# Performance work log

Hardware: AMD Instinct MI355X
Metric: run time of the kernel (lower is better)

## Reference

```python
import jax, jax.numpy as jnp
import numpy as np
from jax import lax

BS, L, D = 512, 200, 128
N_SKILL, N_DIFF, N_HINTS, N_TIME = 1000, 100, 10, 50


def setup_inputs() -> dict:
    key = jax.random.key(0)
    ks = jax.random.split(key, 32)
    s = 1.0 / np.sqrt(D)
    f = jnp.float32
    inp = {
        'skill': jax.random.randint(ks[0], (BS, L), 0, N_SKILL),
        'answer': jax.random.randint(ks[1], (BS, L), 0, 2),
        'diff': jax.random.randint(ks[2], (BS, L), 0, N_DIFF),
        'hints': jax.random.randint(ks[3], (BS, L), 0, N_HINTS),
        'time_used': jax.random.randint(ks[4], (BS, L), 0, N_TIME),
        # embedding tables (padding rows left random; indices never hit them)
        'skill_emb': jax.random.normal(ks[5], (N_SKILL + 2, D), f),
        'answer_emb': jax.random.normal(ks[6], (3, D), f),
        'diff_emb': jax.random.normal(ks[7], (N_DIFF + 2, D), f),
        'hints_emb': jax.random.normal(ks[8], (N_HINTS + 2, D), f),
        'time_emb': jax.random.normal(ks[9], (N_TIME + 2, D), f),
        # Linear weights stored as (in, out): y = x @ W + b
        'Wq2': jax.random.normal(ks[10], (D, D), f) * s,
        'Wk2': jax.random.normal(ks[11], (D, D), f) * s,
        'Wv2': jax.random.normal(ks[12], (D, D), f) * s,
        'Wq3': jax.random.normal(ks[13], (D, D), f) * s,
        'Wk3': jax.random.normal(ks[14], (D, D), f) * s,
        'Wv3': jax.random.normal(ks[15], (D, D), f) * s,
        'fc_W': jax.random.normal(ks[16], (2 * D, D), f) * s,
        'fc_b': jax.random.normal(ks[17], (D,), f) * 0.01,
        'fc2_W': jax.random.normal(ks[18], (2 * D, D), f) * s,
        'fc2_b': jax.random.normal(ks[19], (D,), f) * 0.01,
        'f11_W': jax.random.normal(ks[20], (D, D), f) * s,
        'f11_b': jax.random.normal(ks[21], (D,), f) * 0.01,
        'f12_W': jax.random.normal(ks[22], (D, D), f) * s,
        'f12_b': jax.random.normal(ks[23], (D,), f) * 0.01,
        'f21_W': jax.random.normal(ks[24], (D, D), f) * s,
        'f21_b': jax.random.normal(ks[25], (D,), f) * 0.01,
        'f22_W': jax.random.normal(ks[26], (D, D), f) * s,
        'f22_b': jax.random.normal(ks[27], (D,), f) * 0.01,
    }
    return inp


def _forward(skill, answer, diff, hints, time_used,
             skill_emb, answer_emb, diff_emb, hints_emb, time_emb,
             Wq2, Wk2, Wv2, Wq3, Wk3, Wv3,
             fc_W, fc_b, fc2_W, fc2_b,
             f11_W, f11_b, f12_W, f12_b, f21_W, f21_b, f22_W, f22_b):
    bs = skill.shape[0]
    inv = jnp.asarray(1.0 / np.sqrt(D), skill_emb.dtype)
    es = skill_emb[skill]          # [bs, L, D]
    ed = diff_emb[diff]
    ea = answer_emb[answer]
    eh = hints_emb[hints]
    eu = time_emb[time_used]
    x = jnp.concatenate([es, ed], -1) @ fc_W + fc_b   # [bs, L, D]

    # time-major slices for scan: [L-1, bs, D]
    xs = jnp.swapaxes(x[:, :-1, :], 0, 1)
    xn = jnp.swapaxes(x[:, 1:, :], 0, 1)
    u_t = jnp.swapaxes(eu[:, :-1, :], 0, 1)
    h_t = jnp.swapaxes(eh[:, :-1, :], 0, 1)
    a_t = jnp.swapaxes(ea[:, :-1, :], 0, 1)

    def step(carry, inp):
        h, c = carry
        x_t, x_next, used_t, hints_t, at = inp
        x_t = jnp.concatenate([x_t, h], -1) @ fc2_W + fc2_b
        # branch 1 (W_q_1/W_k_1/W_v_1, used_t) is dead code in the original:
        # out = out_1 + out_2 is immediately overwritten by out = out_2.
        q2 = x_t @ Wq2
        k2 = c @ Wk2
        v2 = hints_t @ Wv2
        out = v2 * jax.nn.sigmoid(q2 * k2 * inv)
        c = jnp.tanh(out @ f11_W + f11_b) * jax.nn.sigmoid(out @ f12_W + f12_b) + c
        q3 = x_t @ Wk3   # note: original swaps W_k_3/W_q_3 names here
        k3 = h @ Wq3
        v3 = at @ Wv3
        o3 = v3 * jax.nn.sigmoid(q3 * k3 * inv)
        h = jnp.tanh(o3 @ f21_W + f21_b) * jax.nn.sigmoid(o3 @ f22_W + f22_b) + c
        y = jax.nn.sigmoid(jnp.sum(x_next * h, axis=-1))  # [bs]
        return (h, c), y

    h0 = jnp.zeros((bs, D), x.dtype)
    c0 = jnp.zeros((bs, D), x.dtype)
    _, ys = lax.scan(step, (h0, c0), (xs, xn, u_t, h_t, a_t))  # ys: [L-1, bs]
    y_pred = jnp.concatenate([ys.T, jnp.zeros((bs, 1), x.dtype)], axis=1)  # [bs, L]
    return y_pred


def reference(skill, answer, diff, hints, time_used,
              skill_emb, answer_emb, diff_emb, hints_emb, time_emb,
              Wq2, Wk2, Wv2, Wq3, Wk3, Wv3,
              fc_W, fc_b, fc2_W, fc2_b,
              f11_W, f11_b, f12_W, f12_b, f21_W, f21_b, f22_W, f22_b):
    return _forward(skill, answer, diff, hints, time_used,
                    skill_emb, answer_emb, diff_emb, hints_emb, time_emb,
                    Wq2, Wk2, Wv2, Wq3, Wk3, Wv3,
                    fc_W, fc_b, fc2_W, fc2_b,
                    f11_W, f11_b, f12_W, f12_b, f21_W, f21_b, f22_W, f22_b)
```

## Files before the change

### kernel.cpp

```cpp
#include <hip/hip_runtime.h>
#include <stdint.h>

typedef unsigned short u16;
typedef unsigned char u8;
typedef unsigned int u32;
typedef unsigned long long u64;

using h8f  = __attribute__((ext_vector_type(8))) _Float16;
using f4_t = __attribute__((ext_vector_type(4))) float;
using l2_t = __attribute__((ext_vector_type(2))) long;

#define MFMAH(a,b,c)  __builtin_amdgcn_mfma_f32_16x16x32_f16((a),(b),(c),0,0,0)
#define MFMAF8(a,b,c) __builtin_amdgcn_mfma_f32_16x16x32_fp8_fp8((a),(b),(c),0,0,0)

#define LO_SCALE 4096.0f
#define LO_INV   0.000244140625f

__device__ __forceinline__ float sigm(float x) {
  return __builtin_amdgcn_rcpf(1.f + __expf(-x));
}
__device__ __forceinline__ float tanh_f(float x) {
  x = fminf(30.f, fmaxf(-30.f, x));
  float e = __expf(-2.f * x);
  return (1.f - e) * __builtin_amdgcn_rcpf(1.f + e);
}
__device__ __forceinline__ u16 f2h_bits(float f) {
  _Float16 h = (_Float16)f;
  union { _Float16 h; u16 u; } v; v.h = h; return v.u;
}
__device__ __forceinline__ float h2f(u16 u) {
  union { _Float16 h; u16 u; } v; v.u = u; return (float)v.h;
}
__device__ __forceinline__ u32 pkrtz(float a, float b) {
  union { __attribute__((ext_vector_type(2))) __fp16 h; u32 u; } v;
  v.h = __builtin_amdgcn_cvt_pkrtz(a, b);
  return v.u;
}
__device__ __forceinline__ u32 pk4f8(float a, float b, float c, float d) {
  u32 r = 0;
  r = __builtin_amdgcn_cvt_pk_fp8_f32(a, b, (int)r, false);
  r = __builtin_amdgcn_cvt_pk_fp8_f32(c, d, (int)r, true);
  return r;
}


__global__ void k_gemm128(const float* __restrict__ A, const float* __restrict__ B,
                          float* __restrict__ C) {
  int g = blockIdx.x * 256 + threadIdx.x;
  int row = g >> 5;
  int c0 = (g & 31) << 2;
  f4_t acc = {0.f, 0.f, 0.f, 0.f};
  for (int k = 0; k < 128; ++k) {
    float a = A[row * 128 + k];
    acc += a * *(const f4_t*)&B[k * 128 + c0];
  }
  *(f4_t*)&C[row * 128 + c0] = acc;
}

__global__ void k_wbig(const float* __restrict__ fc_W, const float* __restrict__ B2,
                       const float* __restrict__ B3, float* __restrict__ WB) {
  int g = blockIdx.x * 256 + threadIdx.x;
  int row = g / 96;
  int j0 = (g % 96) * 4;
  if (j0 < 128) {
    *(f4_t*)&WB[row * 384 + j0] = *(const f4_t*)&fc_W[row * 128 + j0];
  } else {
    const float* Bm = (j0 < 256) ? B2 : B3;
    int jj = j0 & 127;
    f4_t acc = {0.f, 0.f, 0.f, 0.f};
    for (int n = 0; n < 128; ++n)
      acc += fc_W[row * 128 + n] * *(const f4_t*)&Bm[n * 128 + jj];
    *(f4_t*)&WB[row * 384 + j0] = acc;
  }
}

__global__ void k_bbig(const float* __restrict__ fc_b, const float* __restrict__ fc2_b,
                       const float* __restrict__ B2, const float* __restrict__ B3,
                       const float* __restrict__ Wq2, const float* __restrict__ Wk3,
                       float* __restrict__ bb) {
  int j = blockIdx.x * 256 + threadIdx.x;
  if (j >= 384) return;
  if (j < 128) { bb[j] = fc_b[j]; return; }
  const float* Bm = (j < 256) ? B2 : B3;
  const float* Wm = (j < 256) ? Wq2 : Wk3;
  int jj = j & 127;
  float acc = 0.f;
  for (int n = 0; n < 128; ++n)
    acc += fc_b[n] * Bm[n * 128 + jj] + fc2_b[n] * Wm[n * 128 + jj];
  bb[j] = acc;
}

__global__ void k_skdf(const float* __restrict__ skill_emb, const float* __restrict__ diff_emb,
                       const float* __restrict__ WB, const float* __restrict__ bb,
                       float* __restrict__ SK, float* __restrict__ DF) {
  int g = blockIdx.x * 256 + threadIdx.x;
  int row = g / 96, j0 = (g % 96) * 4;
  if (blockIdx.y == 0) {
    if (row >= 1002) return;
    f4_t acc = {0.f, 0.f, 0.f, 0.f};
    for (int d = 0; d < 128; ++d)
      acc += skill_emb[row * 128 + d] * *(const f4_t*)&WB[d * 384 + j0];
    *(f4_t*)&SK[row * 384 + j0] = acc;
  } else {
    if (row >= 102) return;
    f4_t acc = *(const f4_t*)&bb[j0];
    for (int d = 0; d < 128; ++d)
      acc += diff_emb[row * 128 + d] * *(const f4_t*)&WB[(128 + d) * 384 + j0];
    *(f4_t*)&DF[row * 384 + j0] = acc;
  }
}

__global__ void k_tv(const float* __restrict__ hints_emb, const float* __restrict__ Wv2,
                     const float* __restrict__ answer_emb, const float* __restrict__ Wv3,
                     float* __restrict__ Tv2, float* __restrict__ Tv3) {
  int g = blockIdx.x * 256 + threadIdx.x;
  if (g < 384) {
    int i = g >> 5, j0 = (g & 31) << 2;
    f4_t acc = {0.f, 0.f, 0.f, 0.f};
    for (int d = 0; d < 128; ++d)
      acc += hints_emb[i * 128 + d] * *(const f4_t*)&Wv2[d * 128 + j0];
    *(f4_t*)&Tv2[i * 128 + j0] = acc;
  } else if (g < 480) {
    int g2 = g - 384;
    int i = g2 >> 5, j0 = (g2 & 31) << 2;
    f4_t acc = {0.f, 0.f, 0.f, 0.f};
    for (int d = 0; d < 128; ++d)
      acc += answer_emb[i * 128 + d] * *(const f4_t*)&Wv3[d * 128 + j0];
    *(f4_t*)&Tv3[i * 128 + j0] = acc;
  }
}

struct P8 { const float* p[8]; };
__global__ void k_pack(P8 s, u16* __restrict__ whi, u8* __restrict__ wl8) {
  int g = blockIdx.x * 256 + threadIdx.x;
  bool lo = (g >= 16384);
  int gg = g & 16383;
  int m = gg >> 11;
  int r = gg & 2047;
  int ct = (r >> 10) & 1, kk = (r >> 8) & 3, wv = (r >> 6) & 3, l = r & 63;
  const float* src = s.p[m];
  int col = wv * 32 + ct * 16 + (l & 15);
  int kbase = kk * 32 + ((l >> 4) << 3);
  if (!lo) {
    u16 o[8];
    #pragma unroll
    for (int e = 0; e < 8; ++e) o[e] = f2h_bits(src[(kbase + e) * 128 + col]);
    uint4 u;
    u.x = o[0] | ((u32)o[1] << 16); u.y = o[2] | ((u32)o[3] << 16);
    u.z = o[4] | ((u32)o[5] << 16); u.w = o[6] | ((u32)o[7] << 16);
    *(uint4*)(whi + gg * 8) = u;
  } else {
    float lv[8];
    #pragma unroll
    for (int e = 0; e < 8; ++e) {
      float v = src[(kbase + e) * 128 + col];
      lv[e] = (v - (float)((_Float16)v)) * LO_SCALE;
    }
    uint2 u;
    u.x = pk4f8(lv[0], lv[1], lv[2], lv[3]);
    u.y = pk4f8(lv[4], lv[5], lv[6], lv[7]);
    *(uint2*)(wl8 + (size_t)gg * 8) = u;
  }
}


#define RSTRIDE 136
#define RS8 272

__launch_bounds__(256, 1)
__global__ void k_main(const int* __restrict__ skill, const int* __restrict__ answer,
                       const int* __restrict__ diff, const int* __restrict__ hints,
                       const float* __restrict__ SK, const float* __restrict__ DF,
                       const float* __restrict__ Tv2, const float* __restrict__ Tv3,
                       const u16* __restrict__ whi, const u8* __restrict__ wl8,
                       const float* __restrict__ b11p, const float* __restrict__ b12p,
                       const float* __restrict__ b21p, const float* __restrict__ b22p,
                       float* __restrict__ out) {
  __shared__ u16 sh_h[16 * RSTRIDE], sh_hl[16 * RSTRIDE];
  __shared__ u16 sh_c[16 * RSTRIDE], sh_cl[16 * RSTRIDE];
  __shared__ u16 sh_o[16 * RSTRIDE], sh_ol[16 * RSTRIDE];
  __shared__ u16 sh_o3[16 * RSTRIDE], sh_o3l[16 * RSTRIDE];
  __shared__ u8 sh_hc8[16 * RS8];
  __shared__ u8 sh_oo8[16 * RS8];
  __shared__ float sh_red[64];

  const int tid = threadIdx.x;
  const int w = tid >> 6, lane = tid & 63;
  const int row = lane & 15;
  const int fgrp = lane >> 4;
  const int f0a = w * 32 + fgrp * 4;
  const int f0b = f0a + 16;
  const int row_g = blockIdx.x * 16 + row;
  const int r200 = row_g * 200;

  h8f  WH[8][2][4];
  long WL[8][2][4];
  {
    const int base = w * 64 + lane;
    #pragma unroll
    for (int m = 0; m < 8; ++m)
      #pragma unroll
      for (int ct = 0; ct < 2; ++ct)
        #pragma unroll
        for (int kk = 0; kk < 4; ++kk) {
          int f = ((m * 2 + ct) * 4 + kk) * 256 + base;
          WH[m][ct][kk] = *(const h8f*)&whi[(size_t)f * 8];
          WL[m][ct][kk] = *(const long*)&wl8[(size_t)f * 8];
        }
  }

  const f4_t b11A = *(const f4_t*)&b11p[f0a], b11B = *(const f4_t*)&b11p[f0b];
  const f4_t b12A = *(const f4_t*)&b12p[f0a], b12B = *(const f4_t*)&b12p[f0b];
  const f4_t b21A = *(const f4_t*)&b21p[f0a], b21B = *(const f4_t*)&b21p[f0b];
  const f4_t b22A = *(const f4_t*)&b22p[f0a], b22B = *(const f4_t*)&b22p[f0b];

  for (int i = tid; i < 16 * RSTRIDE / 2; i += 256) {
    ((u32*)sh_h)[i] = 0u; ((u32*)sh_c)[i] = 0u;
    ((u32*)sh_hl)[i] = 0u; ((u32*)sh_cl)[i] = 0u;
  }
  for (int i = tid; i < 16 * RS8 / 4; i += 256) ((u32*)sh_hc8)[i] = 0u;
  if (tid < 16) out[(blockIdx.x * 16 + tid) * 200 + 199] = 0.f;

  f4_t cstA = {0.f, 0.f, 0.f, 0.f}, cstB = {0.f, 0.f, 0.f, 0.f};

  int is_cur = skill[r200], id_cur = diff[r200];
  int ih_cur = hints[r200], ia_cur = answer[r200];

  const float inv = 0.088388347648318447f;
  const int rbase = row * RSTRIDE;
  const int widxA = rbase + f0a;
  const int widxB = rbase + f0b;
  int roff[4], boff[4];
  #pragma unroll
  for (int kk = 0; kk < 4; ++kk) {
    roff[kk] = rbase + kk * 32 + fgrp * 8;
    boff[kk] = row * RS8 + (kk * 4 + fgrp) * 16;
  }
  const int jA = w * 4 + (fgrp >> 1);
  const int w8A = row * RS8 + jA * 16 + (fgrp & 1) * 4;
  const int w8B = w8A + 32;

  __syncthreads();

  for (int t = 0; t < 199; ++t) {
    f4_t v2A = *(const f4_t*)&Tv2[ih_cur * 128 + f0a];
    f4_t v2B = *(const f4_t*)&Tv2[ih_cur * 128 + f0b];
    f4_t v3A = *(const f4_t*)&Tv3[ia_cur * 128 + f0a];
    f4_t v3B = *(const f4_t*)&Tv3[ia_cur * 128 + f0b];
    f4_t q2bA = *(const f4_t*)&SK[is_cur * 384 + 128 + f0a]
              + *(const f4_t*)&DF[id_cur * 384 + 128 + f0a];
    f4_t q2bB = *(const f4_t*)&SK[is_cur * 384 + 128 + f0b]
              + *(const f4_t*)&DF[id_cur * 384 + 128 + f0b];
    f4_t q3bA = *(const f4_t*)&SK[is_cur * 384 + 256 + f0a]
              + *(const f4_t*)&DF[id_cur * 384 + 256 + f0a];
    f4_t q3bB = *(const f4_t*)&SK[is_cur * 384 + 256 + f0b]
              + *(const f4_t*)&DF[id_cur * 384 + 256 + f0b];
    int n_s = skill[r200 + t + 1];
    int n_d = diff[r200 + t + 1];
    int n_h = hints[r200 + t + 1];
    int n_a = answer[r200 + t + 1];

    f4_t q2A = {0.f,0.f,0.f,0.f}, q2B = {0.f,0.f,0.f,0.f};
    f4_t q3A = {0.f,0.f,0.f,0.f}, q3B = {0.f,0.f,0.f,0.f};
    f4_t k3A = {0.f,0.f,0.f,0.f}, k3B = {0.f,0.f,0.f,0.f};
    f4_t k2A = {0.f,0.f,0.f,0.f}, k2B = {0.f,0.f,0.f,0.f};
    f4_t lq2A = {0.f,0.f,0.f,0.f}, lq2B = {0.f,0.f,0.f,0.f};
    f4_t lq3A = {0.f,0.f,0.f,0.f}, lq3B = {0.f,0.f,0.f,0.f};
    f4_t lk3A = {0.f,0.f,0.f,0.f}, lk3B = {0.f,0.f,0.f,0.f};
    f4_t lk2A = {0.f,0.f,0.f,0.f}, lk2B = {0.f,0.f,0.f,0.f};
    #pragma unroll
    for (int kk = 0; kk < 4; ++kk) {
      h8f  hh = *(const h8f*)&sh_h[roff[kk]];
      h8f  hl = *(const h8f*)&sh_hl[roff[kk]];
      h8f  ch = *(const h8f*)&sh_c[roff[kk]];
      h8f  cl = *(const h8f*)&sh_cl[roff[kk]];
      l2_t hc = *(const l2_t*)&sh_hc8[boff[kk]];
      long h8 = hc[0], c8 = hc[1];
      q2A = MFMAH(WH[0][0][kk], hh, q2A); q2A = MFMAH(WH[0][0][kk], hl, q2A);
      lq2A = MFMAF8(WL[0][0][kk], h8, lq2A);
      q2B = MFMAH(WH[0][1][kk], hh, q2B); q2B = MFMAH(WH[0][1][kk], hl, q2B);
      lq2B = MFMAF8(WL[0][1][kk], h8, lq2B);
      q3A = MFMAH(WH[1][0][kk], hh, q3A); q3A = MFMAH(WH[1][0][kk], hl, q3A);
      lq3A = MFMAF8(WL[1][0][kk], h8, lq3A);
      q3B = MFMAH(WH[1][1][kk], hh, q3B); q3B = MFMAH(WH[1][1][kk], hl, q3B);
      lq3B = MFMAF8(WL[1][1][kk], h8, lq3B);
      k3A = MFMAH(WH[2][0][kk], hh, k3A); k3A = MFMAH(WH[2][0][kk], hl, k3A);
      lk3A = MFMAF8(WL[2][0][kk], h8, lk3A);
      k3B = MFMAH(WH[2][1][kk], hh, k3B); k3B = MFMAH(WH[2][1][kk], hl, k3B);
      lk3B = MFMAF8(WL[2][1][kk], h8, lk3B);
      k2A = MFMAH(WH[3][0][kk], ch, k2A); k2A = MFMAH(WH[3][0][kk], cl, k2A);
      lk2A = MFMAF8(WL[3][0][kk], c8, lk2A);
      k2B = MFMAH(WH[3][1][kk], ch, k2B); k2B = MFMAH(WH[3][1][kk], cl, k2B);
      lk2B = MFMAF8(WL[3][1][kk], c8, lk2B);
    }

    {
      float ov[4], o3v[4];
      #pragma unroll
      for (int r = 0; r < 4; ++r) {
        float q2v = (q2A[r] + lq2A[r] * LO_INV) + q2bA[r];
        float q3v = (q3A[r] + lq3A[r] * LO_INV) + q3bA[r];
        float k2v = k2A[r] + lk2A[r] * LO_INV;
        float k3v = k3A[r] + lk3A[r] * LO_INV;
        ov[r]  = v2A[r] * sigm(q2v * k2v * inv);
        o3v[r] = v3A[r] * sigm(q3v * k3v * inv);
      }
      uint2 ph; ph.x = pkrtz(ov[0], ov[1]); ph.y = pkrtz(ov[2], ov[3]);
      *(uint2*)&sh_o[widxA] = ph;
      uint2 pl;
      pl.x = pkrtz(ov[0] - h2f((u16)ph.x), ov[1] - h2f((u16)(ph.x >> 16)));
      pl.y = pkrtz(ov[2] - h2f((u16)ph.y), ov[3] - h2f((u16)(ph.y >> 16)));
      *(uint2*)&sh_ol[widxA] = pl;
      uint2 p3; p3.x = pkrtz(o3v[0], o3v[1]); p3.y = pkrtz(o3v[2], o3v[3]);
      *(uint2*)&sh_o3[widxA] = p3;
      uint2 p3l;
      p3l.x = pkrtz(o3v[0] - h2f((u16)p3.x), o3v[1] - h2f((u16)(p3.x >> 16)));
      p3l.y = pkrtz(o3v[2] - h2f((u16)p3.y), o3v[3] - h2f((u16)(p3.y >> 16)));
      *(uint2*)&sh_o3l[widxA] = p3l;
      *(u32*)&sh_oo8[w8A]     = pk4f8(ov[0], ov[1], ov[2], ov[3]);
      *(u32*)&sh_oo8[w8A + 8] = pk4f8(o3v[0], o3v[1], o3v[2], o3v[3]);
    }
    {
      float ov[4], o3v[4];
      #pragma unroll
      for (int r = 0; r < 4; ++r) {
        float q2v = (q2B[r] + lq2B[r] * LO_INV) + q2bB[r];
        float q3v = (q3B[r] + lq3B[r] * LO_INV) + q3bB[r];
        float k2v = k2B[r] + lk2B[r] * LO_INV;
        float k3v = k3B[r] + lk3B[r] * LO_INV;
        ov[r]  = v2B[r] * sigm(q2v * k2v * inv);
        o3v[r] = v3B[r] * sigm(q3v * k3v * inv);
      }
      uint2 ph; ph.x = pkrtz(ov[0], ov[1]); ph.y = pkrtz(ov[2], ov[3]);
      *(uint2*)&sh_o[widxB] = ph;
      uint2 pl;
      pl.x = pkrtz(ov[0] - h2f((u16)ph.x), ov[1] - h2f((u16)(ph.x >> 16)));
      pl.y = pkrtz(ov[2] - h2f((u16)ph.y), ov[3] - h2f((u16)(ph.y >> 16)));
      *(uint2*)&sh_ol[widxB] = pl;
      uint2 p3; p3.x = pkrtz(o3v[0], o3v[1]); p3.y = pkrtz(o3v[2], o3v[3]);
      *(uint2*)&sh_o3[widxB] = p3;
      uint2 p3l;
      p3l.x = pkrtz(o3v[0] - h2f((u16)p3.x), o3v[1] - h2f((u16)(p3.x >> 16)));
      p3l.y = pkrtz(o3v[2] - h2f((u16)p3.y), o3v[3] - h2f((u16)(p3.y >> 16)));
      *(uint2*)&sh_o3l[widxB] = p3l;
      *(u32*)&sh_oo8[w8B]     = pk4f8(ov[0], ov[1], ov[2], ov[3]);
      *(u32*)&sh_oo8[w8B + 8] = pk4f8(o3v[0], o3v[1], o3v[2], o3v[3]);
    }
    __syncthreads();

    f4_t xnA = *(const f4_t*)&SK[n_s * 384 + f0a] + *(const f4_t*)&DF[n_d * 384 + f0a];
    f4_t xnB = *(const f4_t*)&SK[n_s * 384 + f0b] + *(const f4_t*)&DF[n_d * 384 + f0b];

    f4_t a11A = {0.f,0.f,0.f,0.f}, a11B = {0.f,0.f,0.f,0.f};
    f4_t a12A = {0.f,0.f,0.f,0.f}, a12B = {0.f,0.f,0.f,0.f};
    f4_t a21A = {0.f,0.f,0.f,0.f}, a21B = {0.f,0.f,0.f,0.f};
    f4_t a22A = {0.f,0.f,0.f,0.f}, a22B = {0.f,0.f,0.f,0.f};
    f4_t l11A = {0.f,0.f,0.f,0.f}, l11B = {0.f,0.f,0.f,0.f};
    f4_t l12A = {0.f,0.f,0.f,0.f}, l12B = {0.f,0.f,0.f,0.f};
    f4_t l21A = {0.f,0.f,0.f,0.f}, l21B = {0.f,0.f,0.f,0.f};
    f4_t l22A = {0.f,0.f,0.f,0.f}, l22B = {0.f,0.f,0.f,0.f};
    #pragma unroll
    for (int kk = 0; kk < 4; ++kk) {
      h8f  of   = *(const h8f*)&sh_o[roff[kk]];
      h8f  olf  = *(const h8f*)&sh_ol[roff[kk]];
      h8f  o3f  = *(const h8f*)&sh_o3[roff[kk]];
      h8f  o3lf = *(const h8f*)&sh_o3l[roff[kk]];
      l2_t oo = *(const l2_t*)&sh_oo8[boff[kk]];
      long o8 = oo[0], o38 = oo[1];
      a11A = MFMAH(WH[4][0][kk], of, a11A); a11A = MFMAH(WH[4][0][kk], olf, a11A);
      l11A = MFMAF8(WL[4][0][kk], o8, l11A);
      a11B = MFMAH(WH[4][1][kk], of, a11B); a11B = MFMAH(WH[4][1][kk], olf, a11B);
      l11B = MFMAF8(WL[4][1][kk], o8, l11B);
      a12A = MFMAH(WH[5][0][kk], of, a12A); a12A = MFMAH(WH[5][0][kk], olf, a12A);
      l12A = MFMAF8(WL[5][0][kk], o8, l12A);
      a12B = MFMAH(WH[5][1][kk], of, a12B); a12B = MFMAH(WH[5][1][kk], olf, a12B);
      l12B = MFMAF8(WL[5][1][kk], o8, l12B);
      a21A = MFMAH(WH[6][0][kk], o3f, a21A); a21A = MFMAH(WH[6][0][kk], o3lf, a21A);
      l21A = MFMAF8(WL[6][0][kk], o38, l21A);
      a21B = MFMAH(WH[6][1][kk], o3f, a21B); a21B = MFMAH(WH[6][1][kk], o3lf, a21B);
      l21B = MFMAF8(WL[6][1][kk], o38, l21B);
      a22A = MFMAH(WH[7][0][kk], o3f, a22A); a22A = MFMAH(WH[7][0][kk], o3lf, a22A);
      l22A = MFMAF8(WL[7][0][kk], o38, l22A);
      a22B = MFMAH(WH[7][1][kk], o3f, a22B); a22B = MFMAH(WH[7][1][kk], o3lf, a22B);
      l22B = MFMAF8(WL[7][1][kk], o38, l22B);
    }

    float part = 0.f;
    f4_t hvA, hvB;
    #pragma unroll
    for (int r = 0; r < 4; ++r) {
      float a11 = (a11A[r] + l11A[r] * LO_INV) + b11A[r];
      float a12 = (a12A[r] + l12A[r] * LO_INV) + b12A[r];
      float a21 = (a21A[r] + l21A[r] * LO_INV) + b21A[r];
      float a22 = (a22A[r] + l22A[r] * LO_INV) + b22A[r];
      float g = tanh_f(a11) * sigm(a12);
      cstA[r] += g;
      float hh = tanh_f(a21) * sigm(a22) + cstA[r];
      hvA[r] = hh;
      part += xnA[r] * hh;
    }
    #pragma unroll
    for (int r = 0; r < 4; ++r) {
      float a11 = (a11B[r] + l11B[r] * LO_INV) + b11B[r];
      float a12 = (a12B[r] + l12B[r] * LO_INV) + b12B[r];
      float a21 = (a21B[r] + l21B[r] * LO_INV) + b21B[r];
      float a22 = (a22B[r] + l22B[r] * LO_INV) + b22B[r];
      float g = tanh_f(a11) * sigm(a12);
      cstB[r] += g;
      float hh = tanh_f(a21) * sigm(a22) + cstB[r];
      hvB[r] = hh;
      part += xnB[r] * hh;
    }
    part += __shfl_xor(part, 16);
    part += __shfl_xor(part, 32);
    if (lane < 16) sh_red[lane * 4 + w] = part;

    {
      uint2 ph; ph.x = pkrtz(hvA[0], hvA[1]); ph.y = pkrtz(hvA[2], hvA[3]);
      *(uint2*)&sh_h[widxA] = ph;
      uint2 pl;
      pl.x = pkrtz(hvA[0] - h2f((u16)ph.x), hvA[1] - h2f((u16)(ph.x >> 16)));
      pl.y = pkrtz(hvA[2] - h2f((u16)ph.y), hvA[3] - h2f((u16)(ph.y >> 16)));
      *(uint2*)&sh_hl[widxA] = pl;
      uint2 pc; pc.x = pkrtz(cstA[0], cstA[1]); pc.y = pkrtz(cstA[2], cstA[3]);
      *(uint2*)&sh_c[widxA] = pc;
      uint2 pcl;
      pcl.x = pkrtz(cstA[0] - h2f((u16)pc.x), cstA[1] - h2f((u16)(pc.x >> 16)));
      pcl.y = pkrtz(cstA[2] - h2f((u16)pc.y), cstA[3] - h2f((u16)(pc.y >> 16)));
      *(uint2*)&sh_cl[widxA] = pcl;
      *(u32*)&sh_hc8[w8A]     = pk4f8(hvA[0], hvA[1], hvA[2], hvA[3]);
      *(u32*)&sh_hc8[w8A + 8] = pk4f8(cstA[0], cstA[1], cstA[2], cstA[3]);
    }
    {
      uint2 ph; ph.x = pkrtz(hvB[0], hvB[1]); ph.y = pkrtz(hvB[2], hvB[3]);
      *(uint2*)&sh_h[widxB] = ph;
      uint2 pl;
      pl.x = pkrtz(hvB[0] - h2f((u16)ph.x), hvB[1] - h2f((u16)(ph.x >> 16)));
      pl.y = pkrtz(hvB[2] - h2f((u16)ph.y), hvB[3] - h2f((u16)(ph.y >> 16)));
      *(uint2*)&sh_hl[widxB] = pl;
      uint2 pc; pc.x = pkrtz(cstB[0], cstB[1]); pc.y = pkrtz(cstB[2], cstB[3]);
      *(uint2*)&sh_c[widxB] = pc;
      uint2 pcl;
      pcl.x = pkrtz(cstB[0] - h2f((u16)pc.x), cstB[1] - h2f((u16)(pc.x >> 16)));
      pcl.y = pkrtz(cstB[2] - h2f((u16)pc.y), cstB[3] - h2f((u16)(pc.y >> 16)));
      *(uint2*)&sh_cl[widxB] = pcl;
      *(u32*)&sh_hc8[w8B]     = pk4f8(hvB[0], hvB[1], hvB[2], hvB[3]);
      *(u32*)&sh_hc8[w8B + 8] = pk4f8(cstB[0], cstB[1], cstB[2], cstB[3]);
    }

    is_cur = n_s; id_cur = n_d; ih_cur = n_h; ia_cur = n_a;
    __syncthreads();

    if (w == 0 && lane < 16) {
      const f4_t p = *(const f4_t*)&sh_red[lane * 4];
      out[(blockIdx.x * 16 + lane) * 200 + t] = sigm((p[0] + p[1]) + (p[2] + p[3]));
    }
  }
}


extern "C" void kernel_launch(void* const* d_in, const int* in_sizes, int n_in,
                              void* d_out, int out_size, void* d_ws, size_t ws_size,
                              hipStream_t stream) {
  const int* skill  = (const int*)d_in[0];
  const int* answer = (const int*)d_in[1];
  const int* diff   = (const int*)d_in[2];
  const int* hints  = (const int*)d_in[3];
  const float* skill_emb  = (const float*)d_in[5];
  const float* answer_emb = (const float*)d_in[6];
  const float* diff_emb   = (const float*)d_in[7];
  const float* hints_emb  = (const float*)d_in[8];
  const float* Wq2 = (const float*)d_in[10];
  const float* Wk2 = (const float*)d_in[11];
  const float* Wv2 = (const float*)d_in[12];
  const float* Wq3 = (const float*)d_in[13];
  const float* Wk3 = (const float*)d_in[14];
  const float* Wv3 = (const float*)d_in[15];
  const float* fc_W  = (const float*)d_in[16];
  const float* fc_b  = (const float*)d_in[17];
  const float* fc2_W = (const float*)d_in[18];
  const float* fc2_b = (const float*)d_in[19];
  const float* f11_W = (const float*)d_in[20];
  const float* f11_b = (const float*)d_in[21];
  const float* f12_W = (const float*)d_in[22];
  const float* f12_b = (const float*)d_in[23];
  const float* f21_W = (const float*)d_in[24];
  const float* f21_b = (const float*)d_in[25];
  const float* f22_W = (const float*)d_in[26];
  const float* f22_b = (const float*)d_in[27];

  float* ws = (float*)d_ws;
  float* A2 = ws + 0;
  float* A3 = ws + 16384;
  float* B2 = ws + 32768;
  float* B3 = ws + 49152;
  float* WB = ws + 65536;
  float* BB = ws + 163840;
  float* SKt = ws + 164224;
  float* DFt = ws + 548992;
  float* TV2 = ws + 588160;
  float* TV3 = ws + 589696;
  u16* WHI = (u16*)((char*)d_ws + 2360320);
  u8* WL8 = (u8*)d_ws + 2622464;
  float* outp = (float*)d_out;

  k_gemm128<<<16, 256, 0, stream>>>(fc2_W,         Wq2, B2);
  k_gemm128<<<16, 256, 0, stream>>>(fc2_W,         Wk3, B3);
  k_gemm128<<<16, 256, 0, stream>>>(fc2_W + 16384, Wq2, A2);
  k_gemm128<<<16, 256, 0, stream>>>(fc2_W + 16384, Wk3, A3);
  k_wbig<<<96, 256, 0, stream>>>(fc_W, B2, B3, WB);
  k_bbig<<<2, 256, 0, stream>>>(fc_b, fc2_b, B2, B3, Wq2, Wk3, BB);
  k_skdf<<<dim3(376, 2), 256, 0, stream>>>(skill_emb, diff_emb, WB, BB, SKt, DFt);
  k_tv<<<2, 256, 0, stream>>>(hints_emb, Wv2, answer_emb, Wv3, TV2, TV3);
  P8 s;
  s.p[0] = A2; s.p[1] = A3; s.p[2] = Wq3; s.p[3] = Wk2;
  s.p[4] = f11_W; s.p[5] = f12_W; s.p[6] = f21_W; s.p[7] = f22_W;
  k_pack<<<128, 256, 0, stream>>>(s, WHI, WL8);
  k_main<<<32, 256, 0, stream>>>(skill, answer, diff, hints, SKt, DFt, TV2, TV3,
                                 WHI, WL8, f11_b, f12_b, f21_b, f22_b, outp);
}
```

Baseline: 1.246 ms.

## Split recurrent step across 8 waves and stream fp8 low weights from memory

Doubles the block to 512 threads (8 waves), so each wave owns one 16-column tile instead of two. This halves per-wave MFMA chain length per step, and the weight packing is re-laid out to match. The fp8 low-part weights are no longer held in registers; they are reloaded from global/L2 every timestep, along with the biases, to fit register pressure at the higher thread count. The trade is more per-step global loads and a cross-wave reduction over 8 partials, in exchange for more parallel MFMA issue on the latency-bound recurrence.

```diff
diff --git a/kernel.cpp b/kernel.cpp
--- a/kernel.cpp
+++ b/kernel.cpp
@@ -137,9 +137,9 @@
   int gg = g & 16383;
   int m = gg >> 11;
   int r = gg & 2047;
-  int ct = (r >> 10) & 1, kk = (r >> 8) & 3, wv = (r >> 6) & 3, l = r & 63;
+  int kk = r >> 9, w = (r >> 6) & 7, l = r & 63;
   const float* src = s.p[m];
-  int col = wv * 32 + ct * 16 + (l & 15);
+  int col = w * 16 + (l & 15);
   int kbase = kk * 32 + ((l >> 4) << 3);
   if (!lo) {
     u16 o[8];
@@ -167,7 +167,7 @@
 #define RSTRIDE 136
 #define RS8 272
 
-__launch_bounds__(256, 1)
+__launch_bounds__(512, 2)
 __global__ void k_main(const int* __restrict__ skill, const int* __restrict__ answer,
                        const int* __restrict__ diff, const int* __restrict__ hints,
                        const float* __restrict__ SK, const float* __restrict__ DF,
@@ -182,278 +182,203 @@
   __shared__ u16 sh_o3[16 * RSTRIDE], sh_o3l[16 * RSTRIDE];
   __shared__ u8 sh_hc8[16 * RS8];
   __shared__ u8 sh_oo8[16 * RS8];
-  __shared__ float sh_red[64];
+  __shared__ float sh_red[128];
 
   const int tid = threadIdx.x;
   const int w = tid >> 6, lane = tid & 63;
   const int row = lane & 15;
   const int fgrp = lane >> 4;
-  const int f0a = w * 32 + fgrp * 4;
-  const int f0b = f0a + 16;
+  const int f0 = w * 16 + fgrp * 4;
   const int row_g = blockIdx.x * 16 + row;
   const int r200 = row_g * 200;
 
-  h8f  WH[8][2][4];
-  long WL[8][2][4];
+  h8f WH[8][4];
   {
     const int base = w * 64 + lane;
     #pragma unroll
     for (int m = 0; m < 8; ++m)
       #pragma unroll
-      for (int ct = 0; ct < 2; ++ct)
-        #pragma unroll
-        for (int kk = 0; kk < 4; ++kk) {
-          int f = ((m * 2 + ct) * 4 + kk) * 256 + base;
-          WH[m][ct][kk] = *(const h8f*)&whi[(size_t)f * 8];
-          WL[m][ct][kk] = *(const long*)&wl8[(size_t)f * 8];
-        }
-  }
-
-  const f4_t b11A = *(const f4_t*)&b11p[f0a], b11B = *(const f4_t*)&b11p[f0b];
-  const f4_t b12A = *(const f4_t*)&b12p[f0a], b12B = *(const f4_t*)&b12p[f0b];
-  const f4_t b21A = *(const f4_t*)&b21p[f0a], b21B = *(const f4_t*)&b21p[f0b];
-  const f4_t b22A = *(const f4_t*)&b22p[f0a], b22B = *(const f4_t*)&b22p[f0b];
-
-  for (int i = tid; i < 16 * RSTRIDE / 2; i += 256) {
+      for (int kk = 0; kk < 4; ++kk)
+        WH[m][kk] = *(const h8f*)&whi[(size_t)(((m * 4 + kk) * 8 + w) * 64 + lane) * 8];
+  }
+  const u8* wlp = wl8 + (size_t)(w * 64 + lane) * 8;
+
+  for (int i = tid; i < 16 * RSTRIDE / 2; i += 512) {
     ((u32*)sh_h)[i] = 0u; ((u32*)sh_c)[i] = 0u;
     ((u32*)sh_hl)[i] = 0u; ((u32*)sh_cl)[i] = 0u;
   }
-  for (int i = tid; i < 16 * RS8 / 4; i += 256) ((u32*)sh_hc8)[i] = 0u;
+  for (int i = tid; i < 16 * RS8 / 4; i += 512) ((u32*)sh_hc8)[i] = 0u;
   if (tid < 16) out[(blockIdx.x * 16 + tid) * 200 + 199] = 0.f;
 
-  f4_t cstA = {0.f, 0.f, 0.f, 0.f}, cstB = {0.f, 0.f, 0.f, 0.f};
+  f4_t cst = {0.f, 0.f, 0.f, 0.f};
 
   int is_cur = skill[r200], id_cur = diff[r200];
   int ih_cur = hints[r200], ia_cur = answer[r200];
 
   const float inv = 0.088388347648318447f;
   const int rbase = row * RSTRIDE;
-  const int widxA = rbase + f0a;
-  const int widxB = rbase + f0b;
+  const int widx = rbase + f0;
   int roff[4], boff[4];
   #pragma unroll
   for (int kk = 0; kk < 4; ++kk) {
     roff[kk] = rbase + kk * 32 + fgrp * 8;
     boff[kk] = row * RS8 + (kk * 4 + fgrp) * 16;
   }
-  const int jA = w * 4 + (fgrp >> 1);
-  const int w8A = row * RS8 + jA * 16 + (fgrp & 1) * 4;
-  const int w8B = w8A + 32;
+  const int w8 = row * RS8 + (w * 2 + (fgrp >> 1)) * 16 + (fgrp & 1) * 4;
 
   __syncthreads();
 
   for (int t = 0; t < 199; ++t) {
-    f4_t v2A = *(const f4_t*)&Tv2[ih_cur * 128 + f0a];
-    f4_t v2B = *(const f4_t*)&Tv2[ih_cur * 128 + f0b];
-    f4_t v3A = *(const f4_t*)&Tv3[ia_cur * 128 + f0a];
-    f4_t v3B = *(const f4_t*)&Tv3[ia_cur * 128 + f0b];
-    f4_t q2bA = *(const f4_t*)&SK[is_cur * 384 + 128 + f0a]
-              + *(const f4_t*)&DF[id_cur * 384 + 128 + f0a];
-    f4_t q2bB = *(const f4_t*)&SK[is_cur * 384 + 128 + f0b]
-              + *(const f4_t*)&DF[id_cur * 384 + 128 + f0b];
-    f4_t q3bA = *(const f4_t*)&SK[is_cur * 384 + 256 + f0a]
-              + *(const f4_t*)&DF[id_cur * 384 + 256 + f0a];
-    f4_t q3bB = *(const f4_t*)&SK[is_cur * 384 + 256 + f0b]
-              + *(const f4_t*)&DF[id_cur * 384 + 256 + f0b];
+    long wls[4][4];
+    #pragma unroll
+    for (int m = 0; m < 4; ++m)
+      #pragma unroll
+      for (int kk = 0; kk < 4; ++kk)
+        wls[m][kk] = *(const long*)(wlp + (size_t)((m * 4 + kk) * 512) * 8);
+    f4_t v2  = *(const f4_t*)&Tv2[ih_cur * 128 + f0];
+    f4_t v3  = *(const f4_t*)&Tv3[ia_cur * 128 + f0];
+    f4_t q2b = *(const f4_t*)&SK[is_cur * 384 + 128 + f0]
+             + *(const f4_t*)&DF[id_cur * 384 + 128 + f0];
+    f4_t q3b = *(const f4_t*)&SK[is_cur * 384 + 256 + f0]
+             + *(const f4_t*)&DF[id_cur * 384 + 256 + f0];
     int n_s = skill[r200 + t + 1];
     int n_d = diff[r200 + t + 1];
     int n_h = hints[r200 + t + 1];
     int n_a = answer[r200 + t + 1];
 
-    f4_t q2A = {0.f,0.f,0.f,0.f}, q2B = {0.f,0.f,0.f,0.f};
-    f4_t q3A = {0.f,0.f,0.f,0.f}, q3B = {0.f,0.f,0.f,0.f};
-    f4_t k3A = {0.f,0.f,0.f,0.f}, k3B = {0.f,0.f,0.f,0.f};
-    f4_t k2A = {0.f,0.f,0.f,0.f}, k2B = {0.f,0.f,0.f,0.f};
-    f4_t lq2A = {0.f,0.f,0.f,0.f}, lq2B = {0.f,0.f,0.f,0.f};
-    f4_t lq3A = {0.f,0.f,0.f,0.f}, lq3B = {0.f,0.f,0.f,0.f};
-    f4_t lk3A = {0.f,0.f,0.f,0.f}, lk3B = {0.f,0.f,0.f,0.f};
-    f4_t lk2A = {0.f,0.f,0.f,0.f}, lk2B = {0.f,0.f,0.f,0.f};
+    f4_t q2 = {0.f,0.f,0.f,0.f}, q3 = {0.f,0.f,0.f,0.f};
+    f4_t k3 = {0.f,0.f,0.f,0.f}, k2 = {0.f,0.f,0.f,0.f};
     #pragma unroll
     for (int kk = 0; kk < 4; ++kk) {
-      h8f  hh = *(const h8f*)&sh_h[roff[kk]];
-      h8f  hl = *(const h8f*)&sh_hl[roff[kk]];
-      h8f  ch = *(const h8f*)&sh_c[roff[kk]];
-      h8f  cl = *(const h8f*)&sh_cl[roff[kk]];
+      h8f hh = *(const h8f*)&sh_h[roff[kk]];
+      h8f hl = *(const h8f*)&sh_hl[roff[kk]];
+      h8f ch = *(const h8f*)&sh_c[roff[kk]];
+      h8f cl = *(const h8f*)&sh_cl[roff[kk]];
+      q2 = MFMAH(WH[0][kk], hh, q2); q2 = MFMAH(WH[0][kk], hl, q2);
+      q3 = MFMAH(WH[1][kk], hh, q3); q3 = MFMAH(WH[1][kk], hl, q3);
+      k3 = MFMAH(WH[2][kk], hh, k3); k3 = MFMAH(WH[2][kk], hl, k3);
+      k2 = MFMAH(WH[3][kk], ch, k2); k2 = MFMAH(WH[3][kk], cl, k2);
+    }
+    f4_t lq2 = {0.f,0.f,0.f,0.f}, lq3 = {0.f,0.f,0.f,0.f};
+    f4_t lk3 = {0.f,0.f,0.f,0.f}, lk2 = {0.f,0.f,0.f,0.f};
+    #pragma unroll
+    for (int kk = 0; kk < 4; ++kk) {
       l2_t hc = *(const l2_t*)&sh_hc8[boff[kk]];
       long h8 = hc[0], c8 = hc[1];
-      q2A = MFMAH(WH[0][0][kk], hh, q2A); q2A = MFMAH(WH[0][0][kk], hl, q2A);
-      lq2A = MFMAF8(WL[0][0][kk], h8, lq2A);
-      q2B = MFMAH(WH[0][1][kk], hh, q2B); q2B = MFMAH(WH[0][1][kk], hl, q2B);
-      lq2B = MFMAF8(WL[0][1][kk], h8, lq2B);
-      q3A = MFMAH(WH[1][0][kk], hh, q3A); q3A = MFMAH(WH[1][0][kk], hl, q3A);
-      lq3A = MFMAF8(WL[1][0][kk], h8, lq3A);
-      q3B = MFMAH(WH[1][1][kk], hh, q3B); q3B = MFMAH(WH[1][1][kk], hl, q3B);
-      lq3B = MFMAF8(WL[1][1][kk], h8, lq3B);
-      k3A = MFMAH(WH[2][0][kk], hh, k3A); k3A = MFMAH(WH[2][0][kk], hl, k3A);
-      lk3A = MFMAF8(WL[2][0][kk], h8, lk3A);
-      k3B = MFMAH(WH[2][1][kk], hh, k3B); k3B = MFMAH(WH[2][1][kk], hl, k3B);
-      lk3B = MFMAF8(WL[2][1][kk], h8, lk3B);
-      k2A = MFMAH(WH[3][0][kk], ch, k2A); k2A = MFMAH(WH[3][0][kk], cl, k2A);
-      lk2A = MFMAF8(WL[3][0][kk], c8, lk2A);
-      k2B = MFMAH(WH[3][1][kk], ch, k2B); k2B = MFMAH(WH[3][1][kk], cl, k2B);
-      lk2B = MFMAF8(WL[3][1][kk], c8, lk2B);
+      lq2 = MFMAF8(wls[0][kk], h8, lq2);
+      lq3 = MFMAF8(wls[1][kk], h8, lq3);
+      lk3 = MFMAF8(wls[2][kk], h8, lk3);
+      lk2 = MFMAF8(wls[3][kk], c8, lk2);
     }
 
     {
       float ov[4], o3v[4];
       #pragma unroll
       for (int r = 0; r < 4; ++r) {
-        float q2v = (q2A[r] + lq2A[r] * LO_INV) + q2bA[r];
-        float q3v = (q3A[r] + lq3A[r] * LO_INV) + q3bA[r];
-        float k2v = k2A[r] + lk2A[r] * LO_INV;
-        float k3v = k3A[r] + lk3A[r] * LO_INV;
-        ov[r]  = v2A[r] * sigm(q2v * k2v * inv);
-        o3v[r] = v3A[r] * sigm(q3v * k3v * inv);
+        float q2v = (q2[r] + lq2[r] * LO_INV) + q2b[r];
+        float q3v = (q3[r] + lq3[r] * LO_INV) + q3b[r];
+        float k2v = k2[r] + lk2[r] * LO_INV;
+        float k3v = k3[r] + lk3[r] * LO_INV;
+        ov[r]  = v2[r] * sigm(q2v * k2v * inv);
+        o3v[r] = v3[r] * sigm(q3v * k3v * inv);
       }
       uint2 ph; ph.x = pkrtz(ov[0], ov[1]); ph.y = pkrtz(ov[2], ov[3]);
-      *(uint2*)&sh_o[widxA] = ph;
+      *(uint2*)&sh_o[widx] = ph;
       uint2 pl;
       pl.x = pkrtz(ov[0] - h2f((u16)ph.x), ov[1] - h2f((u16)(ph.x >> 16)));
       pl.y = pkrtz(ov[2] - h2f((u16)ph.y), ov[3] - h2f((u16)(ph.y >> 16)));
-      *(uint2*)&sh_ol[widxA] = pl;
+      *(uint2*)&sh_ol[widx] = pl;
       uint2 p3; p3.x = pkrtz(o3v[0], o3v[1]); p3.y = pkrtz(o3v[2], o3v[3]);
-      *(uint2*)&sh_o3[widxA] = p3;
+      *(uint2*)&sh_o3[widx] = p3;
       uint2 p3l;
       p3l.x = pkrtz(o3v[0] - h2f((u16)p3.x), o3v[1] - h2f((u16)(p3.x >> 16)));
       p3l.y = pkrtz(o3v[2] - h2f((u16)p3.y), o3v[3] - h2f((u16)(p3.y >> 16)));
-      *(uint2*)&sh_o3l[widxA] = p3l;
-      *(u32*)&sh_oo8[w8A]     = pk4f8(ov[0], ov[1], ov[2], ov[3]);
-      *(u32*)&sh_oo8[w8A + 8] = pk4f8(o3v[0], o3v[1], o3v[2], o3v[3]);
-    }
-    {
-      float ov[4], o3v[4];
+      *(uint2*)&sh_o3l[widx] = p3l;
+      *(u32*)&sh_oo8[w8]     = pk4f8(ov[0], ov[1], ov[2], ov[3]);
+      *(u32*)&sh_oo8[w8 + 8] = pk4f8(o3v[0], o3v[1], o3v[2], o3v[3]);
+    }
+    __syncthreads();
+
+    long wls2[4][4];
+    #pragma unroll
+    for (int m = 0; m < 4; ++m)
       #pragma unroll
-      for (int r = 0; r < 4; ++r) {
-        float q2v = (q2B[r] + lq2B[r] * LO_INV) + q2bB[r];
-        float q3v = (q3B[r] + lq3B[r] * LO_INV) + q3bB[r];
-        float k2v = k2B[r] + lk2B[r] * LO_INV;
-        float k3v = k3B[r] + lk3B[r] * LO_INV;
-        ov[r]  = v2B[r] * sigm(q2v * k2v * inv);
-        o3v[r] = v3B[r] * sigm(q3v * k3v * inv);
-      }
-      uint2 ph; ph.x = pkrtz(ov[0], ov[1]); ph.y = pkrtz(ov[2], ov[3]);
-      *(uint2*)&sh_o[widxB] = ph;
-      uint2 pl;
-      pl.x = pkrtz(ov[0] - h2f((u16)ph.x), ov[1] - h2f((u16)(ph.x >> 16)));
-      pl.y = pkrtz(ov[2] - h2f((u16)ph.y), ov[3] - h2f((u16)(ph.y >> 16)));
-      *(uint2*)&sh_ol[widxB] = pl;
-      uint2 p3; p3.x = pkrtz(o3v[0], o3v[1]); p3.y = pkrtz(o3v[2], o3v[3]);
-      *(uint2*)&sh_o3[widxB] = p3;
-      uint2 p3l;
-      p3l.x = pkrtz(o3v[0] - h2f((u16)p3.x), o3v[1] - h2f((u16)(p3.x >> 16)));
-      p3l.y = pkrtz(o3v[2] - h2f((u16)p3.y), o3v[3] - h2f((u16)(p3.y >> 16)));
-      *(uint2*)&sh_o3l[widxB] = p3l;
-      *(u32*)&sh_oo8[w8B]     = pk4f8(ov[0], ov[1], ov[2], ov[3]);
-      *(u32*)&sh_oo8[w8B + 8] = pk4f8(o3v[0], o3v[1], o3v[2], o3v[3]);
-    }
-    __syncthreads();
-
-    f4_t xnA = *(const f4_t*)&SK[n_s * 384 + f0a] + *(const f4_t*)&DF[n_d * 384 + f0a];
-    f4_t xnB = *(const f4_t*)&SK[n_s * 384 + f0b] + *(const f4_t*)&DF[n_d * 384 + f0b];
-
-    f4_t a11A = {0.f,0.f,0.f,0.f}, a11B = {0.f,0.f,0.f,0.f};
-    f4_t a12A = {0.f,0.f,0.f,0.f}, a12B = {0.f,0.f,0.f,0.f};
-    f4_t a21A = {0.f,0.f,0.f,0.f}, a21B = {0.f,0.f,0.f,0.f};
-    f4_t a22A = {0.f,0.f,0.f,0.f}, a22B = {0.f,0.f,0.f,0.f};
-    f4_t l11A = {0.f,0.f,0.f,0.f}, l11B = {0.f,0.f,0.f,0.f};
-    f4_t l12A = {0.f,0.f,0.f,0.f}, l12B = {0.f,0.f,0.f,0.f};
-    f4_t l21A = {0.f,0.f,0.f,0.f}, l21B = {0.f,0.f,0.f,0.f};
-    f4_t l22A = {0.f,0.f,0.f,0.f}, l22B = {0.f,0.f,0.f,0.f};
+      for (int kk = 0; kk < 4; ++kk)
+        wls2[m][kk] = *(const long*)(wlp + (size_t)(((m + 4) * 4 + kk) * 512) * 8);
+    f4_t xn = *(const f4_t*)&SK[n_s * 384 + f0] + *(const f4_t*)&DF[n_d * 384 + f0];
+    f4_t b11 = *(const f4_t*)&b11p[f0];
+    f4_t b12 = *(const f4_t*)&b12p[f0];
+    f4_t b21 = *(const f4_t*)&b21p[f0];
+    f4_t b22 = *(const f4_t*)&b22p[f0];
+
+    f4_t a11 = {0.f,0.f,0.f,0.f}, a12 = {0.f,0.f,0.f,0.f};
+    f4_t a21 = {0.f,0.f,0.f,0.f}, a22 = {0.f,0.f,0.f,0.f};
     #pragma unroll
     for (int kk = 0; kk < 4; ++kk) {
-      h8f  of   = *(const h8f*)&sh_o[roff[kk]];
-      h8f  olf  = *(const h8f*)&sh_ol[roff[kk]];
-      h8f  o3f  = *(const h8f*)&sh_o3[roff[kk]];
-      h8f  o3lf = *(const h8f*)&sh_o3l[roff[kk]];
+      h8f of   = *(const h8f*)&sh_o[roff[kk]];
+      h8f olf  = *(const h8f*)&sh_ol[roff[kk]];
+      h8f o3f  = *(const h8f*)&sh_o3[roff[kk]];
+      h8f o3lf = *(const h8f*)&sh_o3l[roff[kk]];
+      a11 = MFMAH(WH[4][kk], of, a11);  a11 = MFMAH(WH[4][kk], olf, a11);
+      a12 = MFMAH(WH[5][kk], of, a12);  a12 = MFMAH(WH[5][kk], olf, a12);
+      a21 = MFMAH(WH[6][kk], o3f, a21); a21 = MFMAH(WH[6][kk], o3lf, a21);
+      a22 = MFMAH(WH[7][kk], o3f, a22); a22 = MFMAH(WH[7][kk], o3lf, a22);
+    }
+    f4_t l11 = {0.f,0.f,0.f,0.f}, l12 = {0.f,0.f,0.f,0.f};
+    f4_t l21 = {0.f,0.f,0.f,0.f}, l22 = {0.f,0.f,0.f,0.f};
+    #pragma unroll
+    for (int kk = 0; kk < 4; ++kk) {
       l2_t oo = *(const l2_t*)&sh_oo8[boff[kk]];
       long o8 = oo[0], o38 = oo[1];
-      a11A = MFMAH(WH[4][0][kk], of, a11A); a11A = MFMAH(WH[4][0][kk], olf, a11A);
-      l11A = MFMAF8(WL[4][0][kk], o8, l11A);
-      a11B = MFMAH(WH[4][1][kk], of, a11B); a11B = MFMAH(WH[4][1][kk], olf, a11B);
-      l11B = MFMAF8(WL[4][1][kk], o8, l11B);
-      a12A = MFMAH(WH[5][0][kk], of, a12A); a12A = MFMAH(WH[5][0][kk], olf, a12A);
-      l12A = MFMAF8(WL[5][0][kk], o8, l12A);
-      a12B = MFMAH(WH[5][1][kk], of, a12B); a12B = MFMAH(WH[5][1][kk], olf, a12B);
-      l12B = MFMAF8(WL[5][1][kk], o8, l12B);
-      a21A = MFMAH(WH[6][0][kk], o3f, a21A); a21A = MFMAH(WH[6][0][kk], o3lf, a21A);
-      l21A = MFMAF8(WL[6][0][kk], o38, l21A);
-      a21B = MFMAH(WH[6][1][kk], o3f, a21B); a21B = MFMAH(WH[6][1][kk], o3lf, a21B);
-      l21B = MFMAF8(WL[6][1][kk], o38, l21B);
-      a22A = MFMAH(WH[7][0][kk], o3f, a22A); a22A = MFMAH(WH[7][0][kk], o3lf, a22A);
-      l22A = MFMAF8(WL[7][0][kk], o38, l22A);
-      a22B = MFMAH(WH[7][1][kk], o3f, a22B); a22B = MFMAH(WH[7][1][kk], o3lf, a22B);
-      l22B = MFMAF8(WL[7][1][kk], o38, l22B);
+      l11 = MFMAF8(wls2[0][kk], o8, l11);
+      l12 = MFMAF8(wls2[1][kk], o8, l12);
+      l21 = MFMAF8(wls2[2][kk], o38, l21);
+      l22 = MFMAF8(wls2[3][kk], o38, l22);
     }
 
     float part = 0.f;
-    f4_t hvA, hvB;
+    f4_t hv;
     #pragma unroll
     for (int r = 0; r < 4; ++r) {
-      float a11 = (a11A[r] + l11A[r] * LO_INV) + b11A[r];
-      float a12 = (a12A[r] + l12A[r] * LO_INV) + b12A[r];
-      float a21 = (a21A[r] + l21A[r] * LO_INV) + b21A[r];
-      float a22 = (a22A[r] + l22A[r] * LO_INV) + b22A[r];
-      float g = tanh_f(a11) * sigm(a12);
-      cstA[r] += g;
-      float hh = tanh_f(a21) * sigm(a22) + cstA[r];
-      hvA[r] = hh;
-      part += xnA[r] * hh;
-    }
-    #pragma unroll
-    for (int r = 0; r < 4; ++r) {
-      float a11 = (a11B[r] + l11B[r] * LO_INV) + b11B[r];
-      float a12 = (a12B[r] + l12B[r] * LO_INV) + b12B[r];
-      float a21 = (a21B[r] + l21B[r] * LO_INV) + b21B[r];
-      float a22 = (a22B[r] + l22B[r] * LO_INV) + b22B[r];
-      float g = tanh_f(a11) * sigm(a12);
-      cstB[r] += g;
-      float hh = tanh_f(a21) * sigm(a22) + cstB[r];
-      hvB[r] = hh;
-      part += xnB[r] * hh;
+      float v11 = (a11[r] + l11[r] * LO_INV) + b11[r];
+      float v12 = (a12[r] + l12[r] * LO_INV) + b12[r];
+      float v21 = (a21[r] + l21[r] * LO_INV) + b21[r];
+      float v22 = (a22[r] + l22[r] * LO_INV) + b22[r];
+      float g = tanh_f(v11) * sigm(v12);
+      cst[r] += g;
+      float hh = tanh_f(v21) * sigm(v22) + cst[r];
+      hv[r] = hh;
+      part += xn[r] * hh;
     }
     part += __shfl_xor(part, 16);
     part += __shfl_xor(part, 32);
-    if (lane < 16) sh_red[lane * 4 + w] = part;
+    if (lane < 16) sh_red[lane * 8 + w] = part;
 
     {
-      uint2 ph; ph.x = pkrtz(hvA[0], hvA[1]); ph.y = pkrtz(hvA[2], hvA[3]);
-      *(uint2*)&sh_h[widxA] = ph;
+      uint2 ph; ph.x = pkrtz(hv[0], hv[1]); ph.y = pkrtz(hv[2], hv[3]);
+      *(uint2*)&sh_h[widx] = ph;
       uint2 pl;
-      pl.x = pkrtz(hvA[0] - h2f((u16)ph.x), hvA[1] - h2f((u16)(ph.x >> 16)));
-      pl.y = pkrtz(hvA[2] - h2f((u16)ph.y), hvA[3] - h2f((u16)(ph.y >> 16)));
-      *(uint2*)&sh_hl[widxA] = pl;
-      uint2 pc; pc.x = pkrtz(cstA[0], cstA[1]); pc.y = pkrtz(cstA[2], cstA[3]);
-      *(uint2*)&sh_c[widxA] = pc;
+      pl.x = pkrtz(hv[0] - h2f((u16)ph.x), hv[1] - h2f((u16)(ph.x >> 16)));
+      pl.y = pkrtz(hv[2] - h2f((u16)ph.y), hv[3] - h2f((u16)(ph.y >> 16)));
+      *(uint2*)&sh_hl[widx] = pl;
+      uint2 pc; pc.x = pkrtz(cst[0], cst[1]); pc.y = pkrtz(cst[2], cst[3]);
+      *(uint2*)&sh_c[widx] = pc;
       uint2 pcl;
-      pcl.x = pkrtz(cstA[0] - h2f((u16)pc.x), cstA[1] - h2f((u16)(pc.x >> 16)));
-      pcl.y = pkrtz(cstA[2] - h2f((u16)pc.y), cstA[3] - h2f((u16)(pc.y >> 16)));
-      *(uint2*)&sh_cl[widxA] = pcl;
-      *(u32*)&sh_hc8[w8A]     = pk4f8(hvA[0], hvA[1], hvA[2], hvA[3]);
-      *(u32*)&sh_hc8[w8A + 8] = pk4f8(cstA[0], cstA[1], cstA[2], cstA[3]);
-    }
-    {
-      uint2 ph; ph.x = pkrtz(hvB[0], hvB[1]); ph.y = pkrtz(hvB[2], hvB[3]);
-      *(uint2*)&sh_h[widxB] = ph;
-      uint2 pl;
-      pl.x = pkrtz(hvB[0] - h2f((u16)ph.x), hvB[1] - h2f((u16)(ph.x >> 16)));
-      pl.y = pkrtz(hvB[2] - h2f((u16)ph.y), hvB[3] - h2f((u16)(ph.y >> 16)));
-      *(uint2*)&sh_hl[widxB] = pl;
-      uint2 pc; pc.x = pkrtz(cstB[0], cstB[1]); pc.y = pkrtz(cstB[2], cstB[3]);
-      *(uint2*)&sh_c[widxB] = pc;
-      uint2 pcl;
-      pcl.x = pkrtz(cstB[0] - h2f((u16)pc.x), cstB[1] - h2f((u16)(pc.x >> 16)));
-      pcl.y = pkrtz(cstB[2] - h2f((u16)pc.y), cstB[3] - h2f((u16)(pc.y >> 16)));
-      *(uint2*)&sh_cl[widxB] = pcl;
-      *(u32*)&sh_hc8[w8B]     = pk4f8(hvB[0], hvB[1], hvB[2], hvB[3]);
-      *(u32*)&sh_hc8[w8B + 8] = pk4f8(cstB[0], cstB[1], cstB[2], cstB[3]);
+      pcl.x = pkrtz(cst[0] - h2f((u16)pc.x), cst[1] - h2f((u16)(pc.x >> 16)));
+      pcl.y = pkrtz(cst[2] - h2f((u16)pc.y), cst[3] - h2f((u16)(pc.y >> 16)));
+      *(uint2*)&sh_cl[widx] = pcl;
+      *(u32*)&sh_hc8[w8]     = pk4f8(hv[0], hv[1], hv[2], hv[3]);
+      *(u32*)&sh_hc8[w8 + 8] = pk4f8(cst[0], cst[1], cst[2], cst[3]);
     }
 
     is_cur = n_s; id_cur = n_d; ih_cur = n_h; ia_cur = n_a;
     __syncthreads();
 
     if (w == 0 && lane < 16) {
-      const f4_t p = *(const f4_t*)&sh_red[lane * 4];
-      out[(blockIdx.x * 16 + lane) * 200 + t] = sigm((p[0] + p[1]) + (p[2] + p[3]));
+      const f4_t p0 = *(const f4_t*)&sh_red[lane * 8];
+      const f4_t p1 = *(const f4_t*)&sh_red[lane * 8 + 4];
+      float s = ((p0[0] + p0[1]) + (p0[2] + p0[3])) + ((p1[0] + p1[1]) + (p1[2] + p1[3]));
+      out[(blockIdx.x * 16 + lane) * 200 + t] = sigm(s);
     }
   }
 }
@@ -516,6 +441,6 @@
   s.p[0] = A2; s.p[1] = A3; s.p[2] = Wq3; s.p[3] = Wk2;
   s.p[4] = f11_W; s.p[5] = f12_W; s.p[6] = f21_W; s.p[7] = f22_W;
   k_pack<<<128, 256, 0, stream>>>(s, WHI, WL8);
-  k_main<<<32, 256, 0, stream>>>(skill, answer, diff, hints, SKt, DFt, TV2, TV3,
+  k_main<<<32, 512, 0, stream>>>(skill, answer, diff, hints, SKt, DFt, TV2, TV3,
                                  WHI, WL8, f11_b, f12_b, f21_b, f22_b, outp);
 }
```

New measurement: 1.212 ms. 1.03x faster.
